# Kernel optimization log

Hardware: AMD Instinct MI355X
Metric: run time of the kernel (lower is better)

The kernel has to match this reference:

```python
import jax, jax.numpy as jnp
import numpy as np
from jax import lax

H = 128  # LSTM hidden size (hardcoded in module)

def setup_inputs() -> dict:
    key = jax.random.key(0)
    ks = jax.random.split(key, 10)
    B, S, D = 256, 512, 80
    T = 3
    s_in = 1.0 / np.sqrt(D)
    s_h = 1.0 / np.sqrt(H)
    return {
        "x": jax.random.normal(ks[0], (B, S, D), dtype=jnp.float32),
        "W_in": jax.random.uniform(ks[1], (256, D), jnp.float32, -s_in, s_in),
        "b_in": jax.random.uniform(ks[2], (256,), jnp.float32, -s_in, s_in),
        "W_ih": jax.random.uniform(ks[3], (4 * H, 256), jnp.float32, -s_h, s_h),
        "b_ih": jax.random.uniform(ks[4], (4 * H,), jnp.float32, -s_h, s_h),
        "W_hh": jax.random.uniform(ks[5], (4 * H, H), jnp.float32, -s_h, s_h),
        "b_hh": jax.random.uniform(ks[6], (4 * H,), jnp.float32, -s_h, s_h),
        "w_time": jax.random.uniform(ks[7], (T,), jnp.float32, -1.0 / np.sqrt(T), 1.0 / np.sqrt(T)),
        "W_br": jax.random.uniform(ks[8], (4, H), jnp.float32, -s_h, s_h),
        "b_br": jax.random.uniform(ks[9], (4,), jnp.float32, -s_h, s_h),
        "batch_size": B,
        "time_steps": T,
    }


def reference(x, W_in, b_in, W_ih, b_ih, W_hh, b_hh, w_time, W_br, b_br, batch_size, time_steps):
    # input projection (dropout is identity in eval mode)
    xl = jnp.einsum('bsd,ed->bse', x, W_in) + b_in  # [B,S,256]
    B, S, _ = xl.shape
    T = time_steps

    def step(carry, inp):
        h, c, h_st, c_st = carry
        xt, i = inp  # xt: [B,256], i: step index
        gates = xt @ W_ih.T + b_ih + h @ W_hh.T + b_hh  # [B,4H]
        ig, fg, gg, og = jnp.split(gates, 4, axis=-1)
        c_new = jax.nn.sigmoid(fg) * c + jax.nn.sigmoid(ig) * jnp.tanh(gg)
        h_new = jax.nn.sigmoid(og) * jnp.tanh(c_new)
        slot = i % T
        oh = jax.nn.one_hot(slot, T, dtype=h_new.dtype)  # [T]
        h_st = h_st * (1.0 - oh) + h_new[:, :, None] * oh  # [B,H,T]
        c_st = c_st * (1.0 - oh) + c_new[:, :, None] * oh
        pool = (slot == T - 1)
        ph = jnp.einsum('bht,t->bh', h_st, w_time)
        pc = jnp.einsum('bht,t->bh', c_st, w_time)
        h_out = jnp.where(pool, ph, h_new)
        c_out = jnp.where(pool, pc, c_new)
        h_st = jnp.where(pool, jnp.zeros_like(h_st), h_st)
        c_st = jnp.where(pool, jnp.zeros_like(c_st), c_st)
        return (h_out, c_out, h_st, c_st), h_out

    init = (jnp.zeros((B, H), xl.dtype), jnp.zeros((B, H), xl.dtype),
            jnp.zeros((B, H, T), xl.dtype), jnp.zeros((B, H, T), xl.dtype))
    _, outs = lax.scan(step, init, (jnp.swapaxes(xl, 0, 1), jnp.arange(S)))
    out = jnp.swapaxes(outs, 0, 1)  # [B,S,H]
    logits = jnp.einsum('bsh,oh->bso', out, W_br) + b_br  # [B,S,4]
    return jax.nn.log_softmax(logits, axis=2)
```

## Files before the change

kernel.cpp:

```cpp
#include <hip/hip_runtime.h>
#include <hip/hip_fp16.h>

#define BB 256
#define SS 512
#define DD 80
#define HH 128
#define GG 512

typedef _Float16 h2_t __attribute__((ext_vector_type(2)));
typedef _Float16 half8 __attribute__((ext_vector_type(8)));
typedef float f32x4 __attribute__((ext_vector_type(4)));

union U32H2 { unsigned int u; h2_t h; unsigned short us[2]; };
union U4H8 { uint4 u; half8 h; };

static __device__ __forceinline__ h2_t u2h(unsigned int u) { U32H2 x; x.u = u; return x.h; }

static __device__ __forceinline__ unsigned int pk2(float a, float b) {
  unsigned int lo = (unsigned int)__half_as_ushort(__float2half(a));
  unsigned int hi = (unsigned int)__half_as_ushort(__float2half(b));
  return (hi << 16) | lo;
}

static __device__ __forceinline__ float fdot2(unsigned int a, unsigned int b, float c) {
#if __has_builtin(__builtin_amdgcn_fdot2)
  return __builtin_amdgcn_fdot2(u2h(a), u2h(b), c, false);
#else
  U32H2 ua, ub; ua.u = a; ub.u = b;
  return c + (float)ua.h[0] * (float)ub.h[0] + (float)ua.h[1] * (float)ub.h[1];
#endif
}

static __device__ __forceinline__ float fsig(float x) {
  return __fdividef(1.f, 1.f + __expf(-x));
}

__global__ __launch_bounds__(128) void prep_kernel(
    const float* __restrict__ W_in, const float* __restrict__ b_in,
    const float* __restrict__ W_ih, const float* __restrict__ b_ih,
    const float* __restrict__ W_hh, const float* __restrict__ b_hh,
    unsigned short* __restrict__ wc16, unsigned short* __restrict__ whh16,
    float* __restrict__ biasc)
{
  const int g = blockIdx.x;
  const int t = threadIdx.x;
  const float* wih = W_ih + g * 256;
  if (t < DD) {
    float s = 0.f;
    for (int e = 0; e < 256; ++e) s += wih[e] * W_in[e * DD + t];
    wc16[g * DD + t] = __half_as_ushort(__float2half(s));
  }
  whh16[g * HH + t] = __half_as_ushort(__float2half(W_hh[g * HH + t]));
  if (t == 0) {
    float s = 0.f;
    for (int e = 0; e < 256; ++e) s += wih[e] * b_in[e];
    biasc[g] = s + b_ih[g] + b_hh[g];
  }
}

__global__ __launch_bounds__(256) void gemm_kernel(
    const float* __restrict__ x,
    const unsigned int* __restrict__ wc,
    uint4* __restrict__ gx)
{
  __shared__ unsigned int Al[64 * 52];
  __shared__ unsigned int Bl[128 * 52];
  const int t  = threadIdx.x;
  const int mt = blockIdx.x;
  const int g0 = blockIdx.y * 128;

  {
    const float4* xr = (const float4*)(x + (size_t)mt * 64 * DD);
    #pragma unroll
    for (int i = 0; i < 5; ++i) {
      int f = t + i * 256;
      int row = f / 20, c4 = f % 20;
      float4 v = xr[row * 20 + c4];
      Al[row * 52 + c4 * 2]     = pk2(v.x, v.y);
      Al[row * 52 + c4 * 2 + 1] = pk2(v.z, v.w);
    }
    #pragma unroll
    for (int i = 0; i < 3; ++i) {
      int f = t + i * 256;
      int row = f / 12, c = f % 12;
      Al[row * 52 + 40 + c] = 0u;
    }
  }
  {
    #pragma unroll
    for (int i = 0; i < 5; ++i) {
      int f = t + i * 256;
      int row = f / 10, c4 = f % 10;
      uint4 v = *(const uint4*)(wc + (size_t)(g0 + row) * 40 + c4 * 4);
      *(uint4*)&Bl[row * 52 + c4 * 4] = v;
    }
    #pragma unroll
    for (int i = 0; i < 6; ++i) {
      int f = t + i * 256;
      int row = f / 12, c = f % 12;
      Bl[row * 52 + 40 + c] = 0u;
    }
  }
  __syncthreads();

  const int w = t >> 6, lane = t & 63;
  const int m = lane & 15, q = lane >> 4;

  half8 af[3];
  #pragma unroll
  for (int kk = 0; kk < 3; ++kk)
    af[kk] = *(const half8*)((const char*)Al + (size_t)(w * 16 + m) * 208 + kk * 64 + q * 16);

  #pragma unroll
  for (int j = 0; j < 8; ++j) {
    f32x4 acc = {0.f, 0.f, 0.f, 0.f};
    #pragma unroll
    for (int kk = 0; kk < 3; ++kk) {
      half8 bf = *(const half8*)((const char*)Bl + (size_t)(j * 16 + m) * 208 + kk * 64 + q * 16);
      acc = __builtin_amdgcn_mfma_f32_16x16x32_f16(af[kk], bf, acc, 0, 0, 0);
    }
    unsigned int lo  = pk2(acc[0], acc[1]);
    unsigned int hi  = pk2(acc[2], acc[3]);
    unsigned int plo = (unsigned int)__shfl_down((int)lo, 16);
    unsigned int phi = (unsigned int)__shfl_down((int)hi, 16);
    if ((q & 1) == 0) {
      const int gl  = g0 + j * 16 + m;
      const int col = ((gl & 127) << 2) | (gl >> 7);
      uint4 o; o.x = lo; o.y = hi; o.z = plo; o.w = phi;
      gx[((size_t)mt * 8 + w * 2 + (q >> 1)) * 512 + (size_t)col] = o;
    }
  }
}

__global__ __attribute__((amdgpu_waves_per_eu(2, 2))) __launch_bounds__(512)
void scan_kernel(
    const uint4* __restrict__ gx,
    const uint4* __restrict__ whh,
    const float* __restrict__ biasc,
    const float* __restrict__ wtime,
    __half* __restrict__ hout)
{
  __shared__ unsigned int hbuf[2][64];
  __shared__ float gbuf[512];
  const int b    = blockIdx.x;
  const int t    = threadIdx.x;
  const int L    = t & 63;
  const int wv   = t >> 6;
  const int q    = t & 3;
  const int hi2  = t >> 2;
  const int g    = q * 128 + hi2;

  half8 af[16];
  {
    const int gr = wv * 64 + (L & 15);
    #pragma unroll
    for (int tt = 0; tt < 4; ++tt) {
      #pragma unroll
      for (int kk = 0; kk < 4; ++kk) {
        U4H8 u;
        u.u = whh[(size_t)(gr + tt * 16) * 16 + kk * 4 + (L >> 4)];
        af[tt * 4 + kk] = u.h;
      }
    }
  }
  #pragma unroll
  for (int i = 0; i < 16; ++i) asm volatile("" : "+v"(af[i]));

  const float bias = biasc[g];
  const float wt0 = wtime[0], wt1 = wtime[1], wt2 = wtime[2];
  if (t < 64) { hbuf[0][t] = 0u; hbuf[1][t] = 0u; }
  float c = 0.f, hst0 = 0.f, hst1 = 0.f, cst0 = 0.f, cst1 = 0.f;
  int slot = 0, s = 0;
  const uint4* gxp = gx + (size_t)b * 64 * 512 + t;
  __syncthreads();

  uint4 gv = gxp[0];
  for (int sb = 0; sb < 64; ++sb) {
    uint4 gn = gv;
    if (sb < 63) gn = gxp[(size_t)(sb + 1) * 512];
    unsigned int ga[4] = {gv.x, gv.y, gv.z, gv.w};
    #pragma unroll 1
    for (int i = 0; i < 8; ++i) {
      const int par = s & 1;
      half8 bf[4];
      #pragma unroll
      for (int kk = 0; kk < 4; ++kk)
        bf[kk] = *(const half8*)((const char*)hbuf[par] + kk * 64 + (L >> 4) * 16);
      #pragma unroll
      for (int tt = 0; tt < 4; ++tt) {
        f32x4 acc = {0.f, 0.f, 0.f, 0.f};
        #pragma unroll
        for (int kk = 0; kk < 4; ++kk)
          acc = __builtin_amdgcn_mfma_f32_16x16x32_f16(af[tt * 4 + kk], bf[kk], acc, 0, 0, 0);
        if ((L & 15) == 0)
          *(f32x4*)&gbuf[wv * 64 + tt * 16 + (L >> 4) * 4] = acc;
      }
      __syncthreads();

      U32H2 gu; gu.u = ga[i >> 1];
      const float gxi = (float)gu.h[i & 1];
      const float d = gbuf[g] + bias + gxi;
      const float din = (q == 2) ? d + d : d;
      const float sv  = fsig(din);
      const float a   = (q == 2) ? 2.f * sv - 1.f : sv;
      const float v1 = __shfl_xor(a, 1);
      const float v2 = __shfl_xor(a, 2);
      const float v3 = __shfl_xor(a, 3);
      const int b0 = q & 1, b1 = q >> 1;
      const float iv = b1 ? (b0 ? v3 : v2) : (b0 ? v1 : a);
      const float fv = b1 ? (b0 ? v2 : v3) : (b0 ? a  : v1);
      const float gg = b1 ? (b0 ? v1 : a ) : (b0 ? v3 : v2);
      const float ov = b1 ? (b0 ? a  : v1) : (b0 ? v2 : v3);
      c = fv * c + iv * gg;
      const float tc = 2.f * fsig(c + c) - 1.f;
      const float hn = ov * tc;
      float hcur;
      if (slot == 2) {
        hcur = hst0 * wt0 + hst1 * wt1 + hn * wt2;
        c    = cst0 * wt0 + cst1 * wt1 + c  * wt2;
        slot = 0;
      } else {
        hcur = hn;
        if (slot == 0) { hst0 = hn; cst0 = c; }
        else           { hst1 = hn; cst1 = c; }
        ++slot;
      }
      if (q == 0) {
        const __half hh2 = __float2half(hcur);
        ((__half*)hbuf[par ^ 1])[hi2] = hh2;
        hout[((size_t)b * SS + s) * HH + hi2] = hh2;
      }
      ++s;
      __syncthreads();
    }
    gv = gn;
  }
}

__global__ __launch_bounds__(256) void out_kernel(
    const uint4* __restrict__ hout,
    const float* __restrict__ Wbr, const float* __restrict__ bbr,
    float4* __restrict__ out)
{
  __shared__ unsigned int wb[4][64];
  __shared__ float bbs[4];
  const int t = threadIdx.x;
  {
    const int o = t >> 6, p = t & 63;
    wb[o][p] = pk2(Wbr[o * HH + 2 * p], Wbr[o * HH + 2 * p + 1]);
  }
  if (t < 4) bbs[t] = bbr[t];
  __syncthreads();

  const size_t row = (size_t)blockIdx.x * 256 + t;
  const uint4* hr = hout + row * 16;
  float a0 = bbs[0], a1 = bbs[1], a2 = bbs[2], a3 = bbs[3];
  #pragma unroll
  for (int qq = 0; qq < 16; ++qq) {
    uint4 hv = hr[qq];
    unsigned int hd[4] = {hv.x, hv.y, hv.z, hv.w};
    #pragma unroll
    for (int d = 0; d < 4; ++d) {
      const int p = qq * 4 + d;
      a0 = fdot2(hd[d], wb[0][p], a0);
      a1 = fdot2(hd[d], wb[1][p], a1);
      a2 = fdot2(hd[d], wb[2][p], a2);
      a3 = fdot2(hd[d], wb[3][p], a3);
    }
  }
  const float m = fmaxf(fmaxf(a0, a1), fmaxf(a2, a3));
  const float e0 = __expf(a0 - m), e1 = __expf(a1 - m), e2 = __expf(a2 - m), e3 = __expf(a3 - m);
  const float lse = m + __logf(e0 + e1 + e2 + e3);
  out[row] = make_float4(a0 - lse, a1 - lse, a2 - lse, a3 - lse);
}

extern "C" void kernel_launch(void* const* d_in, const int* in_sizes, int n_in,
                              void* d_out, int out_size, void* d_ws, size_t ws_size,
                              hipStream_t stream) {
  const float* x     = (const float*)d_in[0];
  const float* W_in  = (const float*)d_in[1];
  const float* b_in  = (const float*)d_in[2];
  const float* W_ih  = (const float*)d_in[3];
  const float* b_ih  = (const float*)d_in[4];
  const float* W_hh  = (const float*)d_in[5];
  const float* b_hh  = (const float*)d_in[6];
  const float* wtime = (const float*)d_in[7];
  const float* W_br  = (const float*)d_in[8];
  const float* b_br  = (const float*)d_in[9];
  (void)in_sizes; (void)n_in; (void)out_size; (void)ws_size;

  char* ws = (char*)d_ws;
  unsigned short* wc16  = (unsigned short*)(ws + 0);
  unsigned short* whh16 = (unsigned short*)(ws + 81920);
  float*          biasc = (float*)(ws + 212992);
  __half*         hout  = (__half*)(ws + 215040);
  uint4*          gx    = (uint4*)(ws + 33769472);

  prep_kernel<<<512, 128, 0, stream>>>(W_in, b_in, W_ih, b_ih, W_hh, b_hh,
                                       wc16, whh16, biasc);
  gemm_kernel<<<dim3(2048, 4), 256, 0, stream>>>(x, (const unsigned int*)wc16, gx);
  scan_kernel<<<256, 512, 0, stream>>>(gx, (const uint4*)whh16, biasc, wtime, hout);
  out_kernel<<<512, 256, 0, stream>>>((const uint4*)hout, W_br, b_br, (float4*)d_out);
}
```

Before: 635.4 us.

## Batch four sequences per scan block using MFMA columns and interleaved gate layout

The scan kernel now handles four batch elements per block (64 blocks instead of 256) by putting four hidden-state vectors into the MFMA B operand columns. W_hh rows and biases are interleaved so each thread reads its four gates from one float4 and computes all gates itself, which removes the cross-lane shuffles. The GEMM kernel is rewritten to load operands straight from global memory into registers and compute all 512 gates per block, writing gx in the new interleaved per-4-batch layout. Barriers become a raw s_waitcnt plus s_barrier, and the inner loop is fully unrolled. The intent is to use more of each MFMA's width per recurrent step, at the cost of only 64 blocks occupying the GPU.

```diff
diff --git a/kernel.cpp b/kernel.cpp
--- a/kernel.cpp
+++ b/kernel.cpp
@@ -35,12 +35,14 @@
   return __fdividef(1.f, 1.f + __expf(-x));
 }
 
+#define BARRIER() asm volatile("s_waitcnt lgkmcnt(0)\n\ts_barrier" ::: "memory")
+
 __global__ __launch_bounds__(128) void prep_kernel(
     const float* __restrict__ W_in, const float* __restrict__ b_in,
     const float* __restrict__ W_ih, const float* __restrict__ b_ih,
     const float* __restrict__ W_hh, const float* __restrict__ b_hh,
-    unsigned short* __restrict__ wc16, unsigned short* __restrict__ whh16,
-    float* __restrict__ biasc)
+    unsigned short* __restrict__ wc16, unsigned short* __restrict__ whhi,
+    float* __restrict__ biasci)
 {
   const int g = blockIdx.x;
   const int t = threadIdx.x;
@@ -50,167 +52,151 @@
     for (int e = 0; e < 256; ++e) s += wih[e] * W_in[e * DD + t];
     wc16[g * DD + t] = __half_as_ushort(__float2half(s));
   }
-  whh16[g * HH + t] = __half_as_ushort(__float2half(W_hh[g * HH + t]));
+  const int a = (g & 127) * 4 + (g >> 7);
+  whhi[a * HH + t] = __half_as_ushort(__float2half(W_hh[g * HH + t]));
   if (t == 0) {
     float s = 0.f;
     for (int e = 0; e < 256; ++e) s += wih[e] * b_in[e];
-    biasc[g] = s + b_ih[g] + b_hh[g];
-  }
-}
-
-__global__ __launch_bounds__(256) void gemm_kernel(
+    biasci[a] = s + b_ih[g] + b_hh[g];
+  }
+}
+
+__global__ __attribute__((amdgpu_waves_per_eu(1, 2))) __launch_bounds__(256)
+void gemm_kernel(
     const float* __restrict__ x,
     const unsigned int* __restrict__ wc,
-    uint4* __restrict__ gx)
-{
-  __shared__ unsigned int Al[64 * 52];
-  __shared__ unsigned int Bl[128 * 52];
-  const int t  = threadIdx.x;
-  const int mt = blockIdx.x;
-  const int g0 = blockIdx.y * 128;
-
+    uint4* __restrict__ gxs)
+{
+  const int t = threadIdx.x, mt = blockIdx.x;
+  const int w = t >> 6, L = t & 63;
+  const int m = L & 15, q4 = L >> 4;
+
+  half8 af[3];
   {
-    const float4* xr = (const float4*)(x + (size_t)mt * 64 * DD);
-    #pragma unroll
-    for (int i = 0; i < 5; ++i) {
-      int f = t + i * 256;
-      int row = f / 20, c4 = f % 20;
-      float4 v = xr[row * 20 + c4];
-      Al[row * 52 + c4 * 2]     = pk2(v.x, v.y);
-      Al[row * 52 + c4 * 2 + 1] = pk2(v.z, v.w);
-    }
-    #pragma unroll
-    for (int i = 0; i < 3; ++i) {
-      int f = t + i * 256;
-      int row = f / 12, c = f % 12;
-      Al[row * 52 + 40 + c] = 0u;
-    }
-  }
-  {
-    #pragma unroll
-    for (int i = 0; i < 5; ++i) {
-      int f = t + i * 256;
-      int row = f / 10, c4 = f % 10;
-      uint4 v = *(const uint4*)(wc + (size_t)(g0 + row) * 40 + c4 * 4);
-      *(uint4*)&Bl[row * 52 + c4 * 4] = v;
-    }
-    #pragma unroll
-    for (int i = 0; i < 6; ++i) {
-      int f = t + i * 256;
-      int row = f / 12, c = f % 12;
-      Bl[row * 52 + 40 + c] = 0u;
-    }
-  }
-  __syncthreads();
-
-  const int w = t >> 6, lane = t & 63;
-  const int m = lane & 15, q = lane >> 4;
-
-  half8 af[3];
-  #pragma unroll
-  for (int kk = 0; kk < 3; ++kk)
-    af[kk] = *(const half8*)((const char*)Al + (size_t)(w * 16 + m) * 208 + kk * 64 + q * 16);
-
-  #pragma unroll
-  for (int j = 0; j < 8; ++j) {
-    f32x4 acc = {0.f, 0.f, 0.f, 0.f};
+    const float* xr = x + (size_t)(mt * 64 + w * 16 + m) * DD;
     #pragma unroll
     for (int kk = 0; kk < 3; ++kk) {
-      half8 bf = *(const half8*)((const char*)Bl + (size_t)(j * 16 + m) * 208 + kk * 64 + q * 16);
-      acc = __builtin_amdgcn_mfma_f32_16x16x32_f16(af[kk], bf, acc, 0, 0, 0);
-    }
-    unsigned int lo  = pk2(acc[0], acc[1]);
-    unsigned int hi  = pk2(acc[2], acc[3]);
-    unsigned int plo = (unsigned int)__shfl_down((int)lo, 16);
-    unsigned int phi = (unsigned int)__shfl_down((int)hi, 16);
-    if ((q & 1) == 0) {
-      const int gl  = g0 + j * 16 + m;
-      const int col = ((gl & 127) << 2) | (gl >> 7);
-      uint4 o; o.x = lo; o.y = hi; o.z = plo; o.w = phi;
-      gx[((size_t)mt * 8 + w * 2 + (q >> 1)) * 512 + (size_t)col] = o;
+      U4H8 u;
+      if (kk < 2 || q4 < 2) {
+        const int k0 = kk * 32 + q4 * 8;
+        float4 f0 = *(const float4*)(xr + k0);
+        float4 f1 = *(const float4*)(xr + k0 + 4);
+        u.u.x = pk2(f0.x, f0.y); u.u.y = pk2(f0.z, f0.w);
+        u.u.z = pk2(f1.x, f1.y); u.u.w = pk2(f1.z, f1.w);
+      } else {
+        u.u.x = 0u; u.u.y = 0u; u.u.z = 0u; u.u.w = 0u;
+      }
+      af[kk] = u.h;
+    }
+  }
+
+  f32x4 acc[32];
+  #pragma unroll
+  for (int j = 0; j < 32; ++j) {
+    f32x4 a = {0.f, 0.f, 0.f, 0.f};
+    const unsigned int* wr = wc + (size_t)(j * 16 + m) * 40 + q4 * 4;
+    #pragma unroll
+    for (int kk = 0; kk < 3; ++kk) {
+      U4H8 u; u.u = *(const uint4*)(wr + kk * 16);
+      a = __builtin_amdgcn_mfma_f32_16x16x32_f16(af[kk], u.h, a, 0, 0, 0);
+    }
+    acc[j] = a;
+  }
+
+  const int b = mt >> 3, nb = b >> 2, cb = b & 3;
+  const int chunk = (mt & 7) * 8 + w * 2 + (q4 >> 1);
+  const int jbase = 2 * (q4 & 1);
+  #pragma unroll
+  for (int d = 0; d < 8; ++d) {
+    const int hidx = d * 16 + m;
+    f32x4 a0 = acc[d], a1 = acc[d + 8], a2 = acc[d + 16], a3 = acc[d + 24];
+    #pragma unroll
+    for (int pr = 0; pr < 2; ++pr) {
+      const int re = pr * 2, ro = re + 1;
+      uint4 o;
+      o.x = pk2(a0[re], a1[re]); o.y = pk2(a2[re], a3[re]);
+      o.z = pk2(a0[ro], a1[ro]); o.w = pk2(a2[ro], a3[ro]);
+      gxs[(size_t)((nb * 64 + chunk) * 4 + jbase + pr) * 512 + cb * 128 + hidx] = o;
     }
   }
 }
 
 __global__ __attribute__((amdgpu_waves_per_eu(2, 2))) __launch_bounds__(512)
 void scan_kernel(
-    const uint4* __restrict__ gx,
-    const uint4* __restrict__ whh,
-    const float* __restrict__ biasc,
+    const uint4* __restrict__ gxs,
+    const uint4* __restrict__ whhi,
+    const float* __restrict__ biasci,
     const float* __restrict__ wtime,
     __half* __restrict__ hout)
 {
-  __shared__ unsigned int hbuf[2][64];
-  __shared__ float gbuf[512];
-  const int b    = blockIdx.x;
-  const int t    = threadIdx.x;
-  const int L    = t & 63;
-  const int wv   = t >> 6;
-  const int q    = t & 3;
-  const int hi2  = t >> 2;
-  const int g    = q * 128 + hi2;
+  __shared__ unsigned int hbuf[2][4 * 68];
+  __shared__ float gbuf[4 * 520];
+  const int nb = blockIdx.x;
+  const int t  = threadIdx.x;
+  const int L  = t & 63;
+  const int wv = t >> 6;
+  const int cb = t >> 7;
+  const int hx = t & 127;
+  const int m  = L & 15, q4 = L >> 4;
+  const int ch = m & 3;
 
   half8 af[16];
-  {
-    const int gr = wv * 64 + (L & 15);
-    #pragma unroll
-    for (int tt = 0; tt < 4; ++tt) {
-      #pragma unroll
-      for (int kk = 0; kk < 4; ++kk) {
-        U4H8 u;
-        u.u = whh[(size_t)(gr + tt * 16) * 16 + kk * 4 + (L >> 4)];
-        af[tt * 4 + kk] = u.h;
-      }
-    }
-  }
+  #pragma unroll
+  for (int tt = 0; tt < 4; ++tt)
+    #pragma unroll
+    for (int kk = 0; kk < 4; ++kk) {
+      U4H8 u; u.u = whhi[(size_t)(wv * 64 + tt * 16 + m) * 16 + kk * 4 + q4];
+      af[tt * 4 + kk] = u.h;
+    }
   #pragma unroll
   for (int i = 0; i < 16; ++i) asm volatile("" : "+v"(af[i]));
 
-  const float bias = biasc[g];
+  const float4 bias4 = *(const float4*)&biasci[hx * 4];
   const float wt0 = wtime[0], wt1 = wtime[1], wt2 = wtime[2];
-  if (t < 64) { hbuf[0][t] = 0u; hbuf[1][t] = 0u; }
+  if (t < 272) { hbuf[0][t] = 0u; hbuf[1][t] = 0u; }
   float c = 0.f, hst0 = 0.f, hst1 = 0.f, cst0 = 0.f, cst1 = 0.f;
   int slot = 0, s = 0;
-  const uint4* gxp = gx + (size_t)b * 64 * 512 + t;
+  const size_t bglob = (size_t)nb * 4 + cb;
+  const uint4* gp = gxs + (size_t)nb * 256 * 512 + t;
   __syncthreads();
 
-  uint4 gv = gxp[0];
+  uint4 gxv[4], gxn[4];
+  #pragma unroll
+  for (int j = 0; j < 4; ++j) gxv[j] = gp[(size_t)j * 512];
   for (int sb = 0; sb < 64; ++sb) {
-    uint4 gn = gv;
-    if (sb < 63) gn = gxp[(size_t)(sb + 1) * 512];
-    unsigned int ga[4] = {gv.x, gv.y, gv.z, gv.w};
-    #pragma unroll 1
+    #pragma unroll
+    for (int j = 0; j < 4; ++j)
+      gxn[j] = (sb < 63) ? gp[(size_t)((sb + 1) * 4 + j) * 512] : gxv[j];
+    #pragma unroll
     for (int i = 0; i < 8; ++i) {
       const int par = s & 1;
       half8 bf[4];
       #pragma unroll
       for (int kk = 0; kk < 4; ++kk)
-        bf[kk] = *(const half8*)((const char*)hbuf[par] + kk * 64 + (L >> 4) * 16);
+        bf[kk] = *(const half8*)&hbuf[par][ch * 68 + kk * 16 + q4 * 4];
       #pragma unroll
       for (int tt = 0; tt < 4; ++tt) {
-        f32x4 acc = {0.f, 0.f, 0.f, 0.f};
-        #pragma unroll
-        for (int kk = 0; kk < 4; ++kk)
-          acc = __builtin_amdgcn_mfma_f32_16x16x32_f16(af[tt * 4 + kk], bf[kk], acc, 0, 0, 0);
-        if ((L & 15) == 0)
-          *(f32x4*)&gbuf[wv * 64 + tt * 16 + (L >> 4) * 4] = acc;
-      }
-      __syncthreads();
-
-      U32H2 gu; gu.u = ga[i >> 1];
-      const float gxi = (float)gu.h[i & 1];
-      const float d = gbuf[g] + bias + gxi;
-      const float din = (q == 2) ? d + d : d;
-      const float sv  = fsig(din);
-      const float a   = (q == 2) ? 2.f * sv - 1.f : sv;
-      const float v1 = __shfl_xor(a, 1);
-      const float v2 = __shfl_xor(a, 2);
-      const float v3 = __shfl_xor(a, 3);
-      const int b0 = q & 1, b1 = q >> 1;
-      const float iv = b1 ? (b0 ? v3 : v2) : (b0 ? v1 : a);
-      const float fv = b1 ? (b0 ? v2 : v3) : (b0 ? a  : v1);
-      const float gg = b1 ? (b0 ? v1 : a ) : (b0 ? v3 : v2);
-      const float ov = b1 ? (b0 ? a  : v1) : (b0 ? v2 : v3);
+        f32x4 a0 = {0.f, 0.f, 0.f, 0.f}, a1 = {0.f, 0.f, 0.f, 0.f};
+        a0 = __builtin_amdgcn_mfma_f32_16x16x32_f16(af[tt * 4 + 0], bf[0], a0, 0, 0, 0);
+        a1 = __builtin_amdgcn_mfma_f32_16x16x32_f16(af[tt * 4 + 1], bf[1], a1, 0, 0, 0);
+        a0 = __builtin_amdgcn_mfma_f32_16x16x32_f16(af[tt * 4 + 2], bf[2], a0, 0, 0, 0);
+        a1 = __builtin_amdgcn_mfma_f32_16x16x32_f16(af[tt * 4 + 3], bf[3], a1, 0, 0, 0);
+        f32x4 acc = a0 + a1;
+        if (m < 4)
+          *(f32x4*)&gbuf[m * 520 + (wv * 16 + tt * 4 + q4) * 4] = acc;
+      }
+      BARRIER();
+      const float4 g4 = *(const float4*)&gbuf[cb * 520 + hx * 4];
+      const uint4 gw = gxv[i >> 1];
+      U32H2 u0, u1;
+      u0.u = (i & 1) ? gw.z : gw.x;
+      u1.u = (i & 1) ? gw.w : gw.y;
+      const float pi = g4.x + bias4.x + (float)u0.h[0];
+      const float pf = g4.y + bias4.y + (float)u0.h[1];
+      const float pg = g4.z + bias4.z + (float)u1.h[0];
+      const float po = g4.w + bias4.w + (float)u1.h[1];
+      const float iv = fsig(pi), fv = fsig(pf), ov = fsig(po);
+      const float gg = 2.f * fsig(pg + pg) - 1.f;
       c = fv * c + iv * gg;
       const float tc = 2.f * fsig(c + c) - 1.f;
       const float hn = ov * tc;
@@ -225,15 +211,18 @@
         else           { hst1 = hn; cst1 = c; }
         ++slot;
       }
-      if (q == 0) {
-        const __half hh2 = __float2half(hcur);
-        ((__half*)hbuf[par ^ 1])[hi2] = hh2;
-        hout[((size_t)b * SS + s) * HH + hi2] = hh2;
+      const unsigned int hu  = (unsigned int)__half_as_ushort(__float2half(hcur));
+      const unsigned int hup = (unsigned int)__shfl_down((int)hu, 1);
+      if (!(t & 1)) {
+        const unsigned int pkh = (hup << 16) | (hu & 0xffffu);
+        hbuf[par ^ 1][cb * 68 + (hx >> 1)] = pkh;
+        *(unsigned int*)((char*)hout + ((bglob * SS + s) * HH + hx) * 2) = pkh;
       }
       ++s;
-      __syncthreads();
-    }
-    gv = gn;
+      BARRIER();
+    }
+    #pragma unroll
+    for (int j = 0; j < 4; ++j) gxv[j] = gxn[j];
   }
 }
 
@@ -268,9 +257,9 @@
       a3 = fdot2(hd[d], wb[3][p], a3);
     }
   }
-  const float m = fmaxf(fmaxf(a0, a1), fmaxf(a2, a3));
-  const float e0 = __expf(a0 - m), e1 = __expf(a1 - m), e2 = __expf(a2 - m), e3 = __expf(a3 - m);
-  const float lse = m + __logf(e0 + e1 + e2 + e3);
+  const float mx = fmaxf(fmaxf(a0, a1), fmaxf(a2, a3));
+  const float e0 = __expf(a0 - mx), e1 = __expf(a1 - mx), e2 = __expf(a2 - mx), e3 = __expf(a3 - mx);
+  const float lse = mx + __logf(e0 + e1 + e2 + e3);
   out[row] = make_float4(a0 - lse, a1 - lse, a2 - lse, a3 - lse);
 }
 
@@ -290,15 +279,15 @@
   (void)in_sizes; (void)n_in; (void)out_size; (void)ws_size;
 
   char* ws = (char*)d_ws;
-  unsigned short* wc16  = (unsigned short*)(ws + 0);
-  unsigned short* whh16 = (unsigned short*)(ws + 81920);
-  float*          biasc = (float*)(ws + 212992);
-  __half*         hout  = (__half*)(ws + 215040);
-  uint4*          gx    = (uint4*)(ws + 33769472);
+  unsigned short* wc16   = (unsigned short*)(ws + 0);
+  unsigned short* whhi   = (unsigned short*)(ws + 81920);
+  float*          biasci = (float*)(ws + 212992);
+  __half*         hout   = (__half*)(ws + 215040);
+  uint4*          gxs    = (uint4*)(ws + 33769472);
 
   prep_kernel<<<512, 128, 0, stream>>>(W_in, b_in, W_ih, b_ih, W_hh, b_hh,
-                                       wc16, whh16, biasc);
-  gemm_kernel<<<dim3(2048, 4), 256, 0, stream>>>(x, (const unsigned int*)wc16, gx);
-  scan_kernel<<<256, 512, 0, stream>>>(gx, (const uint4*)whh16, biasc, wtime, hout);
+                                       wc16, whhi, biasci);
+  gemm_kernel<<<2048, 256, 0, stream>>>(x, (const unsigned int*)wc16, gxs);
+  scan_kernel<<<64, 512, 0, stream>>>(gxs, (const uint4*)whhi, biasci, wtime, hout);
   out_kernel<<<512, 256, 0, stream>>>((const uint4*)hout, W_br, b_br, (float4*)d_out);
 }
```

New measurement: 833.4 us. 31.2% more time.
